# Performance work log

Hardware: AMD Instinct MI355X
Metric: run time of the kernel (lower is better)

## Reference

```python
import jax, jax.numpy as jnp
import numpy as np

B, S, D = 4, 2048, 1024
ATTN_D, OUT_D, H = 1024, 1024, 16
EPS = 1e-12


def setup_inputs() -> dict:
    key = jax.random.key(0)
    ks = jax.random.split(key, 9)
    s = 0.02
    return {
        "x": jax.random.normal(ks[0], (B, S, D), dtype=jnp.float32),
        "wq": jax.random.normal(ks[1], (D, ATTN_D), dtype=jnp.float32) * s,
        "bq": jnp.zeros((ATTN_D,), dtype=jnp.float32),
        "wk": jax.random.normal(ks[2], (D, ATTN_D), dtype=jnp.float32) * s,
        "bk": jnp.zeros((ATTN_D,), dtype=jnp.float32),
        "wv": jax.random.normal(ks[3], (D, ATTN_D), dtype=jnp.float32) * s,
        "bv": jnp.zeros((ATTN_D,), dtype=jnp.float32),
        "wo": jax.random.normal(ks[4], (ATTN_D, OUT_D), dtype=jnp.float32) * s,
        "bo": jnp.zeros((OUT_D,), dtype=jnp.float32),
        "ln_g": jnp.ones((OUT_D,), dtype=jnp.float32),
        "ln_b": jnp.zeros((OUT_D,), dtype=jnp.float32),
    }


def reference(x, wq, bq, wk, bk, wv, bv, wo, bo, ln_g, ln_b):
    b, s, _ = x.shape
    hd = ATTN_D // H  # head_dim
    # projections -> [B, H, S, hd]
    q = (x @ wq + bq).reshape(b, s, H, hd).transpose(0, 2, 1, 3)
    k = (x @ wk + bk).reshape(b, s, H, hd).transpose(0, 2, 1, 3)
    v = (x @ wv + bv).reshape(b, s, H, hd).transpose(0, 2, 1, 3)
    # full O(S^2) score matrix, as in the original module
    scores = jnp.einsum("bhqd,bhkd->bhqk", q, k) / jnp.sqrt(jnp.float32(hd))
    attn = jax.nn.softmax(scores, axis=-1)
    out = jnp.einsum("bhqk,bhkd->bhqd", attn, v)
    out = out.transpose(0, 2, 1, 3).reshape(b, s, ATTN_D)
    out = out @ wo + bo
    # LayerNorm (no residual in this module)
    mu = jnp.mean(out, axis=-1, keepdims=True)
    var = jnp.var(out, axis=-1, keepdims=True)
    out = (out - mu) * jax.lax.rsqrt(var + EPS) * ln_g + ln_b
    return out
```

## Files before the change

kernel.cpp:

```cpp
#include <hip/hip_runtime.h>

typedef __bf16 bf16;
typedef __bf16 bf16x4 __attribute__((ext_vector_type(4)));
typedef __bf16 bf16x8 __attribute__((ext_vector_type(8)));
typedef float f32x4 __attribute__((ext_vector_type(4)));

#define NB 4
#define NS 2048
#define ND 1024
#define NH 16
#define HD 64

#define QSCALE 0.18033688f

__device__ __forceinline__ void gload_lds16(const void* g, void* l) {
  __builtin_amdgcn_global_load_lds(
      (const __attribute__((address_space(1))) void*)g,
      (__attribute__((address_space(3))) void*)l, 16, 0, 0);
}

__device__ __forceinline__ float fast_exp2(float x) {
#if __has_builtin(__builtin_amdgcn_exp2f)
  return __builtin_amdgcn_exp2f(x);
#else
  return exp2f(x);
#endif
}

__global__ __launch_bounds__(256) void k_cvt(const float* __restrict__ src,
                                             bf16* __restrict__ dst) {
  size_t i = ((size_t)blockIdx.x * 256 + threadIdx.x) * 4;
  float4 v = *(const float4*)(src + i);
  bf16x4 o = {(__bf16)v.x, (__bf16)v.y, (__bf16)v.z, (__bf16)v.w};
  *(bf16x4*)(dst + i) = o;
}

__global__ __launch_bounds__(256) void k_cvt_T(const float* __restrict__ src,
                                               bf16* __restrict__ dst) {
  __shared__ float t[32][33];
  int tx = threadIdx.x, ty = threadIdx.y;
  int x = blockIdx.x * 32 + tx;
  int y = blockIdx.y * 32 + ty;
#pragma unroll
  for (int j = 0; j < 4; ++j)
    t[ty + j * 8][tx] = src[(size_t)(y + j * 8) * 1024 + x];
  __syncthreads();
  int x2 = blockIdx.y * 32 + tx;
  int y2 = blockIdx.x * 32 + ty;
#pragma unroll
  for (int j = 0; j < 4; ++j)
    dst[(size_t)(y2 + j * 8) * 1024 + x2] = (__bf16)t[tx][ty + j * 8];
}

__device__ __forceinline__ void gemm_mainloop(const bf16* __restrict__ A,
                                              const bf16* __restrict__ BT,
                                              int bm, int bn, int K,
                                              bf16* sA, bf16* sB,
                                              f32x4 acc[4][4]) {
  const int tid = threadIdx.x;
  const int w = tid >> 6, lane = tid & 63, quad = lane >> 4, l15 = lane & 15;
  const int wm = (w >> 1) * 64, wn = (w & 1) * 64;
  const bf16* ga = A + (size_t)(bm * 128 + (tid >> 2)) * K + (tid & 3) * 8;
  const bf16* gb = BT + (size_t)(bn * 128 + (tid >> 2)) * K + (tid & 3) * 8;
  bf16* lA0 = sA + w * 512;
  bf16* lA1 = sA + 2048 + w * 512;
  bf16* lB0 = sB + w * 512;
  bf16* lB1 = sB + 2048 + w * 512;
  const int kiter = K >> 5;
  for (int kt = 0; kt < kiter; ++kt) {
    gload_lds16(ga, lA0);
    gload_lds16(ga + (size_t)64 * K, lA1);
    gload_lds16(gb, lB0);
    gload_lds16(gb + (size_t)64 * K, lB1);
    ga += 32;
    gb += 32;
    __syncthreads();
    bf16x8 av[4], bv[4];
#pragma unroll
    for (int i = 0; i < 4; ++i)
      av[i] = *(const bf16x8*)(sA + (wm + i * 16 + l15) * 32 + quad * 8);
#pragma unroll
    for (int i = 0; i < 4; ++i)
      bv[i] = *(const bf16x8*)(sB + (wn + i * 16 + l15) * 32 + quad * 8);
#pragma unroll
    for (int mi = 0; mi < 4; ++mi)
#pragma unroll
      for (int ni = 0; ni < 4; ++ni)
        acc[mi][ni] = __builtin_amdgcn_mfma_f32_16x16x32_bf16(
            av[mi], bv[ni], acc[mi][ni], 0, 0, 0);
    __syncthreads();
  }
}

__global__ __launch_bounds__(256) void k_gemm_qkv(
    const bf16* __restrict__ A, const bf16* __restrict__ BT,
    const float* __restrict__ bq, const float* __restrict__ bk,
    const float* __restrict__ bv, bf16* __restrict__ Q, bf16* __restrict__ K,
    bf16* __restrict__ V) {
  __shared__ alignas(16) bf16 sA[4096];
  __shared__ alignas(16) bf16 sB[4096];
  f32x4 acc[4][4] = {};
  const int bm = blockIdx.y, bn = blockIdx.x;
  gemm_mainloop(A, BT, bm, bn, 1024, sA, sB, acc);
  const int tid = threadIdx.x;
  const int w = tid >> 6, lane = tid & 63, quad = lane >> 4, l15 = lane & 15;
  const int wm = (w >> 1) * 64, wn = (w & 1) * 64;
#pragma unroll
  for (int ni = 0; ni < 4; ++ni) {
    int col = bn * 128 + wn + ni * 16 + l15;
    int which = col >> 10, nn = col & 1023;
    int h = nn >> 6, d = nn & 63;
    const float* bias = which == 0 ? bq : which == 1 ? bk : bv;
    bf16* dst = which == 0 ? Q : which == 1 ? K : V;
    float bb = bias[nn];
    float scl = which == 0 ? QSCALE : 1.f;
#pragma unroll
    for (int mi = 0; mi < 4; ++mi) {
      int row = bm * 128 + wm + mi * 16 + quad * 4;
#pragma unroll
      for (int r = 0; r < 4; ++r) {
        int rr = row + r;
        int b = rr >> 11, s = rr & 2047;
        __bf16 val = (__bf16)((acc[mi][ni][r] + bb) * scl);
        if (which == 2)
          dst[(((size_t)b * NH + h) * HD + d) * NS + s] = val;
        else
          dst[(((size_t)b * NH + h) * NS + s) * HD + d] = val;
      }
    }
  }
}

__global__ __launch_bounds__(256) void k_gemm_out(const bf16* __restrict__ A,
                                                  const bf16* __restrict__ BT,
                                                  const float* __restrict__ bo,
                                                  float* __restrict__ Y) {
  __shared__ alignas(16) bf16 sA[4096];
  __shared__ alignas(16) bf16 sB[4096];
  f32x4 acc[4][4] = {};
  const int bm = blockIdx.y, bn = blockIdx.x;
  gemm_mainloop(A, BT, bm, bn, 1024, sA, sB, acc);
  const int tid = threadIdx.x;
  const int w = tid >> 6, lane = tid & 63, quad = lane >> 4, l15 = lane & 15;
  const int wm = (w >> 1) * 64, wn = (w & 1) * 64;
#pragma unroll
  for (int ni = 0; ni < 4; ++ni) {
    int col = bn * 128 + wn + ni * 16 + l15;
    float bb = bo[col];
#pragma unroll
    for (int mi = 0; mi < 4; ++mi) {
      int row = bm * 128 + wm + mi * 16 + quad * 4;
#pragma unroll
      for (int r = 0; r < 4; ++r)
        Y[(size_t)(row + r) * 1024 + col] = acc[mi][ni][r] + bb;
    }
  }
}

__global__ __launch_bounds__(256, 4) void k_attn(const bf16* __restrict__ Qg,
                                                 const bf16* __restrict__ Kg,
                                                 const bf16* __restrict__ VtG,
                                                 bf16* __restrict__ O) {
  __shared__ alignas(16) char smem[24576];
  bf16* sK = (bf16*)smem;
  bf16* sVt = (bf16*)(smem + 16384);
  const int tid = threadIdx.x;
  const int w = tid >> 6, lane = tid & 63, quad = lane >> 4, l15 = lane & 15;
  const int l7 = l15 & 7, l8 = lane >> 3;
  const int bh = blockIdx.x >> 4;
  const int qt = blockIdx.x & 15;
  const bf16* Qh = Qg + (size_t)bh * NS * HD;
  const bf16* Kh = Kg + (size_t)bh * NS * HD;
  const bf16* Vh = VtG + (size_t)bh * HD * NS;
  bf16* Pw = (bf16*)smem + w * 2048;

  const int q0 = qt * 128 + w * 32;
  bf16x8 qb[2][2];
#pragma unroll
  for (int ni = 0; ni < 2; ++ni)
#pragma unroll
    for (int ks = 0; ks < 2; ++ks)
      qb[ni][ks] = *(const bf16x8*)(Qh + (size_t)(q0 + ni * 16 + l15) * HD +
                                    ks * 32 + quad * 8);

  const int gsw = ((lane & 7) ^ l8) * 8;
  const bf16* gk = Kh + (size_t)(w * 8 + l8) * HD + gsw;
  const bf16* gv = Vh + (size_t)(w * 8 + l8) * NS + gsw;
  bf16* dk0 = sK + w * 512;
  bf16* dk1 = sK + (4 + w) * 512;
  bf16* dv0 = sVt + w * 512;
  bf16* dv1 = sVt + (4 + w) * 512;

  f32x4 o_acc[4][2] = {};
  float l_run[2] = {0.f, 0.f};

  int offA[4][2], offV[4][2], offP[2][2];
#pragma unroll
  for (int mi = 0; mi < 4; ++mi)
#pragma unroll
    for (int ks = 0; ks < 2; ++ks) {
      offA[mi][ks] = (mi * 16 + l15) * 64 + (((ks * 4 + quad) ^ l7) * 8);
      offV[mi][ks] = offA[mi][ks];
    }
#pragma unroll
  for (int ks = 0; ks < 2; ++ks)
#pragma unroll
    for (int ni = 0; ni < 2; ++ni)
      offP[ks][ni] = (ni * 16 + l15) * 64 + (((ks * 4 + quad) ^ l7) * 8);

  for (int c = 0; c < NS; c += 64) {
    __syncthreads();
    gload_lds16(gk, dk0);
    gload_lds16(gk + 32 * HD, dk1);
    gload_lds16(gv, dv0);
    gload_lds16(gv + 32 * NS, dv1);
    gk += 64 * HD;
    gv += 64;
    __syncthreads();

    f32x4 s[4][2] = {};
#pragma unroll
    for (int ks = 0; ks < 2; ++ks)
#pragma unroll
      for (int mi = 0; mi < 4; ++mi) {
        bf16x8 ak = *(const bf16x8*)(sK + offA[mi][ks]);
#pragma unroll
        for (int ni = 0; ni < 2; ++ni)
          s[mi][ni] = __builtin_amdgcn_mfma_f32_16x16x32_bf16(
              ak, qb[ni][ks], s[mi][ni], 0, 0, 0);
      }
    __syncthreads();

    float t0 = 0.f, t1 = 0.f;
#pragma unroll
    for (int mi = 0; mi < 4; ++mi)
#pragma unroll
      for (int r = 0; r < 4; ++r) {
        s[mi][0][r] = fast_exp2(s[mi][0][r]);
        t0 += s[mi][0][r];
        s[mi][1][r] = fast_exp2(s[mi][1][r]);
        t1 += s[mi][1][r];
      }
    t0 += __shfl_xor(t0, 16, 64);
    t0 += __shfl_xor(t0, 32, 64);
    t1 += __shfl_xor(t1, 16, 64);
    t1 += __shfl_xor(t1, 32, 64);
    l_run[0] += t0;
    l_run[1] += t1;

#pragma unroll
    for (int ni = 0; ni < 2; ++ni)
#pragma unroll
      for (int mi = 0; mi < 4; ++mi) {
        bf16x4 p = {(__bf16)s[mi][ni][0], (__bf16)s[mi][ni][1],
                    (__bf16)s[mi][ni][2], (__bf16)s[mi][ni][3]};
        *(bf16x4*)(Pw + (ni * 16 + l15) * 64 +
                   (((2 * mi + (quad >> 1)) ^ l7) * 8) + (quad & 1) * 4) = p;
      }

#pragma unroll
    for (int ks = 0; ks < 2; ++ks) {
      bf16x8 pb[2];
#pragma unroll
      for (int ni = 0; ni < 2; ++ni)
        pb[ni] = *(const bf16x8*)(Pw + offP[ks][ni]);
#pragma unroll
      for (int mi = 0; mi < 4; ++mi) {
        bf16x8 av = *(const bf16x8*)(sVt + offV[mi][ks]);
#pragma unroll
        for (int ni = 0; ni < 2; ++ni)
          o_acc[mi][ni] = __builtin_amdgcn_mfma_f32_16x16x32_bf16(
              av, pb[ni], o_acc[mi][ni], 0, 0, 0);
      }
    }
  }

  int b = bh >> 4, h = bh & 15;
#pragma unroll
  for (int ni = 0; ni < 2; ++ni) {
    float inv = 1.f / l_run[ni];
    int q = q0 + ni * 16 + l15;
    size_t orow = ((size_t)b * NS + q) * 1024 + h * 64;
#pragma unroll
    for (int mi = 0; mi < 4; ++mi) {
      bf16x4 ov = {
          (__bf16)(o_acc[mi][ni][0] * inv), (__bf16)(o_acc[mi][ni][1] * inv),
          (__bf16)(o_acc[mi][ni][2] * inv), (__bf16)(o_acc[mi][ni][3] * inv)};
      *(bf16x4*)(O + orow + mi * 16 + quad * 4) = ov;
    }
  }
}

__global__ __launch_bounds__(256) void k_ln(float* __restrict__ Y,
                                            const float* __restrict__ g,
                                            const float* __restrict__ bta) {
  int row = blockIdx.x, tid = threadIdx.x;
  float4 v = ((const float4*)(Y + (size_t)row * 1024))[tid];
  float sm = v.x + v.y + v.z + v.w;
  float sq = v.x * v.x + v.y * v.y + v.z * v.z + v.w * v.w;
#pragma unroll
  for (int off = 1; off < 64; off <<= 1) {
    sm += __shfl_xor(sm, off, 64);
    sq += __shfl_xor(sq, off, 64);
  }
  __shared__ float red[8];
  int w = tid >> 6, lane = tid & 63;
  if (lane == 0) {
    red[w] = sm;
    red[4 + w] = sq;
  }
  __syncthreads();
  sm = red[0] + red[1] + red[2] + red[3];
  sq = red[4] + red[5] + red[6] + red[7];
  float mu = sm * (1.f / 1024.f);
  float var = sq * (1.f / 1024.f) - mu * mu;
  float rstd = rsqrtf(var + 1e-12f);
  float4 g4 = ((const float4*)g)[tid];
  float4 b4 = ((const float4*)bta)[tid];
  float4 o;
  o.x = (v.x - mu) * rstd * g4.x + b4.x;
  o.y = (v.y - mu) * rstd * g4.y + b4.y;
  o.z = (v.z - mu) * rstd * g4.z + b4.z;
  o.w = (v.w - mu) * rstd * g4.w + b4.w;
  ((float4*)(Y + (size_t)row * 1024))[tid] = o;
}

extern "C" void kernel_launch(void* const* d_in, const int* in_sizes, int n_in,
                              void* d_out, int out_size, void* d_ws,
                              size_t ws_size, hipStream_t stream) {
  const float* x = (const float*)d_in[0];
  const float* wq = (const float*)d_in[1];
  const float* bq = (const float*)d_in[2];
  const float* wk = (const float*)d_in[3];
  const float* bk = (const float*)d_in[4];
  const float* wv = (const float*)d_in[5];
  const float* bv = (const float*)d_in[6];
  const float* wo = (const float*)d_in[7];
  const float* bo = (const float*)d_in[8];
  const float* ln_g = (const float*)d_in[9];
  const float* ln_b = (const float*)d_in[10];
  float* out = (float*)d_out;

  char* ws = (char*)d_ws;
  bf16* xb = (bf16*)ws;          ws += 16777216;
  bf16* wqkvT = (bf16*)ws;       ws += 6291456;
  bf16* woT = (bf16*)ws;         ws += 2097152;
  bf16* Qh = (bf16*)ws;          ws += 16777216;
  bf16* Kh = (bf16*)ws;          ws += 16777216;
  bf16* Vt = (bf16*)ws;          ws += 16777216;
  bf16* AOb = (bf16*)ws;         ws += 16777216;

  k_cvt<<<8192, 256, 0, stream>>>(x, xb);
  dim3 tb(32, 8);
  k_cvt_T<<<dim3(32, 32), tb, 0, stream>>>(wq, wqkvT);
  k_cvt_T<<<dim3(32, 32), tb, 0, stream>>>(wk, wqkvT + 1024 * 1024);
  k_cvt_T<<<dim3(32, 32), tb, 0, stream>>>(wv, wqkvT + 2 * 1024 * 1024);
  k_cvt_T<<<dim3(32, 32), tb, 0, stream>>>(wo, woT);

  k_gemm_qkv<<<dim3(24, 64), 256, 0, stream>>>(xb, wqkvT, bq, bk, bv, Qh, Kh,
                                               Vt);
  k_attn<<<NB * NH * (NS / 128), 256, 0, stream>>>(Qh, Kh, Vt, AOb);
  k_gemm_out<<<dim3(8, 64), 256, 0, stream>>>(AOb, woT, bo, out);
  k_ln<<<8192, 256, 0, stream>>>(out, ln_g, ln_b);
}
```

Before: 328.4 us.

## Enlarge attention query tile and move V transpose to a separate kernel

The attention kernel now gives each wave 64 queries instead of 32, so each block covers 256 queries. This halves the number of K/V tile reloads per head and the per-tile barrier count, and P gets its own LDS region, which removes one sync. The row-sum shuffles are deferred to the epilogue. The QKV GEMM now writes V in row layout instead of a strided scattered transpose, and a new k_vT kernel transposes it through LDS. The cost is more registers and LDS per block (occupancy hint 4→2), an extra launch, and an extra V buffer round trip through memory.

After: 308.4 us. -6.1%, faster.

```diff
diff --git a/kernel.cpp b/kernel.cpp
--- a/kernel.cpp
+++ b/kernel.cpp
@@ -50,6 +50,34 @@
 #pragma unroll
   for (int j = 0; j < 4; ++j)
     dst[(size_t)(y2 + j * 8) * 1024 + x2] = (__bf16)t[tx][ty + j * 8];
+}
+
+__global__ __launch_bounds__(256) void k_vT(const bf16* __restrict__ V,
+                                            bf16* __restrict__ Vt) {
+  __shared__ bf16 t[64][72];
+  int tid = threadIdx.x;
+  int bh = blockIdx.x >> 5, st = blockIdx.x & 31;
+  const bf16* src = V + ((size_t)bh * NS + st * 64) * HD;
+#pragma unroll
+  for (int rep = 0; rep < 2; ++rep) {
+    int idx = rep * 256 + tid;
+    int r = idx >> 3, c8 = (idx & 7) * 8;
+    *(bf16x8*)&t[r][c8] = *(const bf16x8*)(src + (size_t)r * HD + c8);
+  }
+  __syncthreads();
+  bf16* dst = Vt + (size_t)bh * HD * NS + st * 64;
+#pragma unroll
+  for (int rep = 0; rep < 2; ++rep) {
+    int idx = rep * 256 + tid;
+    int d = idx >> 3, s8 = (idx & 7) * 8;
+    bf16x8 v;
+#pragma unroll
+    for (int j = 0; j < 8; ++j) {
+      int jj = (j + tid) & 7;
+      v[jj] = t[s8 + jj][d];
+    }
+    *(bf16x8*)(dst + (size_t)d * NS + s8) = v;
+  }
 }
 
 __device__ __forceinline__ void gemm_mainloop(const bf16* __restrict__ A,
@@ -121,11 +149,8 @@
       for (int r = 0; r < 4; ++r) {
         int rr = row + r;
         int b = rr >> 11, s = rr & 2047;
-        __bf16 val = (__bf16)((acc[mi][ni][r] + bb) * scl);
-        if (which == 2)
-          dst[(((size_t)b * NH + h) * HD + d) * NS + s] = val;
-        else
-          dst[(((size_t)b * NH + h) * NS + s) * HD + d] = val;
+        dst[(((size_t)b * NH + h) * NS + s) * HD + d] =
+            (__bf16)((acc[mi][ni][r] + bb) * scl);
       }
     }
   }
@@ -157,27 +182,27 @@
   }
 }
 
-__global__ __launch_bounds__(256, 4) void k_attn(const bf16* __restrict__ Qg,
+__global__ __launch_bounds__(256, 2) void k_attn(const bf16* __restrict__ Qg,
                                                  const bf16* __restrict__ Kg,
                                                  const bf16* __restrict__ VtG,
                                                  bf16* __restrict__ O) {
-  __shared__ alignas(16) char smem[24576];
+  __shared__ alignas(16) char smem[49152];
   bf16* sK = (bf16*)smem;
-  bf16* sVt = (bf16*)(smem + 16384);
+  bf16* sVt = (bf16*)(smem + 8192);
   const int tid = threadIdx.x;
   const int w = tid >> 6, lane = tid & 63, quad = lane >> 4, l15 = lane & 15;
   const int l7 = l15 & 7, l8 = lane >> 3;
-  const int bh = blockIdx.x >> 4;
-  const int qt = blockIdx.x & 15;
+  const int bh = blockIdx.x >> 3;
+  const int qt = blockIdx.x & 7;
   const bf16* Qh = Qg + (size_t)bh * NS * HD;
   const bf16* Kh = Kg + (size_t)bh * NS * HD;
   const bf16* Vh = VtG + (size_t)bh * HD * NS;
-  bf16* Pw = (bf16*)smem + w * 2048;
-
-  const int q0 = qt * 128 + w * 32;
-  bf16x8 qb[2][2];
-#pragma unroll
-  for (int ni = 0; ni < 2; ++ni)
+  bf16* Pw = (bf16*)(smem + 16384) + w * 4096;
+
+  const int q0 = qt * 256 + w * 64;
+  bf16x8 qb[4][2];
+#pragma unroll
+  for (int ni = 0; ni < 4; ++ni)
 #pragma unroll
     for (int ks = 0; ks < 2; ++ks)
       qb[ni][ks] = *(const bf16x8*)(Qh + (size_t)(q0 + ni * 16 + l15) * HD +
@@ -191,21 +216,19 @@
   bf16* dv0 = sVt + w * 512;
   bf16* dv1 = sVt + (4 + w) * 512;
 
-  f32x4 o_acc[4][2] = {};
-  float l_run[2] = {0.f, 0.f};
-
-  int offA[4][2], offV[4][2], offP[2][2];
+  f32x4 o_acc[4][4] = {};
+  float l_run[4] = {0.f, 0.f, 0.f, 0.f};
+
+  int offA[4][2], offP[2][4];
 #pragma unroll
   for (int mi = 0; mi < 4; ++mi)
 #pragma unroll
-    for (int ks = 0; ks < 2; ++ks) {
+    for (int ks = 0; ks < 2; ++ks)
       offA[mi][ks] = (mi * 16 + l15) * 64 + (((ks * 4 + quad) ^ l7) * 8);
-      offV[mi][ks] = offA[mi][ks];
-    }
 #pragma unroll
   for (int ks = 0; ks < 2; ++ks)
 #pragma unroll
-    for (int ni = 0; ni < 2; ++ni)
+    for (int ni = 0; ni < 4; ++ni)
       offP[ks][ni] = (ni * 16 + l15) * 64 + (((ks * 4 + quad) ^ l7) * 8);
 
   for (int c = 0; c < NS; c += 64) {
@@ -218,57 +241,42 @@
     gv += 64;
     __syncthreads();
 
-    f32x4 s[4][2] = {};
-#pragma unroll
-    for (int ks = 0; ks < 2; ++ks)
-#pragma unroll
-      for (int mi = 0; mi < 4; ++mi) {
+#pragma unroll
+    for (int mi = 0; mi < 4; ++mi) {
+      f32x4 s[4] = {};
+#pragma unroll
+      for (int ks = 0; ks < 2; ++ks) {
         bf16x8 ak = *(const bf16x8*)(sK + offA[mi][ks]);
 #pragma unroll
-        for (int ni = 0; ni < 2; ++ni)
-          s[mi][ni] = __builtin_amdgcn_mfma_f32_16x16x32_bf16(
-              ak, qb[ni][ks], s[mi][ni], 0, 0, 0);
+        for (int ni = 0; ni < 4; ++ni)
+          s[ni] = __builtin_amdgcn_mfma_f32_16x16x32_bf16(ak, qb[ni][ks],
+                                                          s[ni], 0, 0, 0);
       }
-    __syncthreads();
-
-    float t0 = 0.f, t1 = 0.f;
-#pragma unroll
-    for (int mi = 0; mi < 4; ++mi)
-#pragma unroll
-      for (int r = 0; r < 4; ++r) {
-        s[mi][0][r] = fast_exp2(s[mi][0][r]);
-        t0 += s[mi][0][r];
-        s[mi][1][r] = fast_exp2(s[mi][1][r]);
-        t1 += s[mi][1][r];
-      }
-    t0 += __shfl_xor(t0, 16, 64);
-    t0 += __shfl_xor(t0, 32, 64);
-    t1 += __shfl_xor(t1, 16, 64);
-    t1 += __shfl_xor(t1, 32, 64);
-    l_run[0] += t0;
-    l_run[1] += t1;
-
-#pragma unroll
-    for (int ni = 0; ni < 2; ++ni)
-#pragma unroll
-      for (int mi = 0; mi < 4; ++mi) {
-        bf16x4 p = {(__bf16)s[mi][ni][0], (__bf16)s[mi][ni][1],
-                    (__bf16)s[mi][ni][2], (__bf16)s[mi][ni][3]};
+#pragma unroll
+      for (int ni = 0; ni < 4; ++ni) {
+#pragma unroll
+        for (int r = 0; r < 4; ++r) {
+          s[ni][r] = fast_exp2(s[ni][r]);
+          l_run[ni] += s[ni][r];
+        }
+        bf16x4 p = {(__bf16)s[ni][0], (__bf16)s[ni][1], (__bf16)s[ni][2],
+                    (__bf16)s[ni][3]};
         *(bf16x4*)(Pw + (ni * 16 + l15) * 64 +
                    (((2 * mi + (quad >> 1)) ^ l7) * 8) + (quad & 1) * 4) = p;
       }
+    }
 
 #pragma unroll
     for (int ks = 0; ks < 2; ++ks) {
-      bf16x8 pb[2];
-#pragma unroll
-      for (int ni = 0; ni < 2; ++ni)
+      bf16x8 pb[4];
+#pragma unroll
+      for (int ni = 0; ni < 4; ++ni)
         pb[ni] = *(const bf16x8*)(Pw + offP[ks][ni]);
 #pragma unroll
       for (int mi = 0; mi < 4; ++mi) {
-        bf16x8 av = *(const bf16x8*)(sVt + offV[mi][ks]);
-#pragma unroll
-        for (int ni = 0; ni < 2; ++ni)
+        bf16x8 av = *(const bf16x8*)(sVt + offA[mi][ks]);
+#pragma unroll
+        for (int ni = 0; ni < 4; ++ni)
           o_acc[mi][ni] = __builtin_amdgcn_mfma_f32_16x16x32_bf16(
               av, pb[ni], o_acc[mi][ni], 0, 0, 0);
       }
@@ -277,8 +285,11 @@
 
   int b = bh >> 4, h = bh & 15;
 #pragma unroll
-  for (int ni = 0; ni < 2; ++ni) {
-    float inv = 1.f / l_run[ni];
+  for (int ni = 0; ni < 4; ++ni) {
+    float l = l_run[ni];
+    l += __shfl_xor(l, 16, 64);
+    l += __shfl_xor(l, 32, 64);
+    float inv = 1.f / l;
     int q = q0 + ni * 16 + l15;
     size_t orow = ((size_t)b * NS + q) * 1024 + h * 64;
 #pragma unroll
@@ -347,6 +358,7 @@
   bf16* woT = (bf16*)ws;         ws += 2097152;
   bf16* Qh = (bf16*)ws;          ws += 16777216;
   bf16* Kh = (bf16*)ws;          ws += 16777216;
+  bf16* Vh = (bf16*)ws;          ws += 16777216;
   bf16* Vt = (bf16*)ws;          ws += 16777216;
   bf16* AOb = (bf16*)ws;         ws += 16777216;
 
@@ -358,8 +370,9 @@
   k_cvt_T<<<dim3(32, 32), tb, 0, stream>>>(wo, woT);
 
   k_gemm_qkv<<<dim3(24, 64), 256, 0, stream>>>(xb, wqkvT, bq, bk, bv, Qh, Kh,
-                                               Vt);
-  k_attn<<<NB * NH * (NS / 128), 256, 0, stream>>>(Qh, Kh, Vt, AOb);
+                                               Vh);
+  k_vT<<<NB * NH * 32, 256, 0, stream>>>(Vh, Vt);
+  k_attn<<<NB * NH * (NS / 256), 256, 0, stream>>>(Qh, Kh, Vt, AOb);
   k_gemm_out<<<dim3(8, 64), 256, 0, stream>>>(AOb, woT, bo, out);
   k_ln<<<8192, 256, 0, stream>>>(out, ln_g, ln_b);
 }
```
